# Optimization experiments

Hardware: AMD Instinct MI355X
Metric: run time of the kernel (lower is better)

The kernel has to match this reference:

```python
import jax, jax.numpy as jnp
import numpy as np

N = 50000      # num_nodes
E = 800000     # edges (before self loops)
IN = 64        # in_dim
H = 128        # hidden_node_dim
DH = 256       # decoder_and_message_hidden_dim
L = 3          # propagation_steps


def _lin(key, fan_in, fan_out):
    s = 1.0 / np.sqrt(fan_in)
    return jax.random.uniform(key, (fan_in, fan_out), jnp.float32, -s, s)


def setup_inputs() -> dict:
    key = jax.random.key(0)
    ks = iter(jax.random.split(key, 40))
    x = jax.random.normal(next(ks), (N, IN), jnp.float32)
    edge_index = jax.random.randint(next(ks), (2, E), 0, N, jnp.int64)
    enc_W = _lin(next(ks), IN, H); enc_b = jnp.zeros((H,), jnp.float32)
    # message MLP: Linear(2H->DH) tanh, Linear(DH->DH) tanh, Linear(DH->H)
    msg_W0 = jnp.stack([_lin(next(ks), 2 * H, DH) for _ in range(L)])
    msg_b0 = jnp.zeros((L, DH), jnp.float32)
    msg_W1 = jnp.stack([_lin(next(ks), DH, DH) for _ in range(L)])
    msg_b1 = jnp.zeros((L, DH), jnp.float32)
    msg_W2 = jnp.stack([_lin(next(ks), DH, H) for _ in range(L)])
    msg_b2 = jnp.zeros((L, H), jnp.float32)
    # GRUCell params, torch layout [3H, H] chunks (r, z, n)
    gru_Wih = jnp.stack([_lin(next(ks), H, 3 * H).T for _ in range(L)])
    gru_Whh = jnp.stack([_lin(next(ks), H, 3 * H).T for _ in range(L)])
    gru_bih = jnp.zeros((L, 3 * H), jnp.float32)
    gru_bhh = jnp.zeros((L, 3 * H), jnp.float32)
    # decoder: Linear(H->DH) tanh, Linear(DH->DH) tanh, Linear(DH->1)
    dec_W0 = _lin(next(ks), H, DH); dec_b0 = jnp.zeros((DH,), jnp.float32)
    dec_W1 = _lin(next(ks), DH, DH); dec_b1 = jnp.zeros((DH,), jnp.float32)
    dec_W2 = _lin(next(ks), DH, 1); dec_b2 = jnp.zeros((1,), jnp.float32)
    return dict(x=x, edge_index=edge_index, enc_W=enc_W, enc_b=enc_b,
                msg_W0=msg_W0, msg_b0=msg_b0, msg_W1=msg_W1, msg_b1=msg_b1,
                msg_W2=msg_W2, msg_b2=msg_b2, gru_Wih=gru_Wih, gru_Whh=gru_Whh,
                gru_bih=gru_bih, gru_bhh=gru_bhh, dec_W0=dec_W0, dec_b0=dec_b0,
                dec_W1=dec_W1, dec_b1=dec_b1, dec_W2=dec_W2, dec_b2=dec_b2)


def reference(x, edge_index, enc_W, enc_b, msg_W0, msg_b0, msg_W1, msg_b1,
              msg_W2, msg_b2, gru_Wih, gru_Whh, gru_bih, gru_bhh,
              dec_W0, dec_b0, dec_W1, dec_b1, dec_W2, dec_b2):
    n = x.shape[0]
    # add self loops (PyG add_self_loops appends (v, v))
    loops = jnp.arange(n, dtype=edge_index.dtype)
    src = jnp.concatenate([edge_index[0], loops])  # j (source)
    dst = jnp.concatenate([edge_index[1], loops])  # i (target)
    counts = jax.ops.segment_sum(jnp.ones_like(dst, jnp.float32), dst, num_segments=n)
    h = jnp.tanh(x @ enc_W + enc_b)                # encoder [N, H]
    for l in range(L):
        # message: f([x_i || x_j]) per edge
        m = jnp.concatenate([h[dst], h[src]], axis=-1)            # [E+N, 2H]
        m = jnp.tanh(m @ msg_W0[l] + msg_b0[l])
        m = jnp.tanh(m @ msg_W1[l] + msg_b1[l])
        m = m @ msg_W2[l] + msg_b2[l]                              # [E+N, H]
        aggr = jax.ops.segment_sum(m, dst, num_segments=n) / counts[:, None]
        # GRUCell(input=aggr, hidden=h)
        gi = aggr @ gru_Wih[l].T + gru_bih[l]                      # [N, 3H]
        gh = h @ gru_Whh[l].T + gru_bhh[l]
        i_r, i_z, i_n = jnp.split(gi, 3, axis=-1)
        h_r, h_z, h_n = jnp.split(gh, 3, axis=-1)
        r = jax.nn.sigmoid(i_r + h_r)
        z = jax.nn.sigmoid(i_z + h_z)
        nn_ = jnp.tanh(i_n + r * h_n)
        h = (1.0 - z) * nn_ + z * h
    # decoder
    y = jnp.tanh(h @ dec_W0 + dec_b0)
    y = jnp.tanh(y @ dec_W1 + dec_b1)
    y = y @ dec_W2 + dec_b2                                        # [N, 1]
    return y.reshape(-1, n)[0]                                     # view(-1, N).squeeze(0)
```

## Files before the change

### kernel.cpp

```cpp
#include <hip/hip_runtime.h>

typedef __bf16 bf16x8 __attribute__((ext_vector_type(8)));
typedef float  f32x4  __attribute__((ext_vector_type(4)));

__device__ inline unsigned short f2bf(float f){
  unsigned int u = __float_as_uint(f);
  return (unsigned short)((u + 0x7fffu + ((u >> 16) & 1u)) >> 16);
}
__device__ inline float tanh_fast(float x){
  float e = __builtin_amdgcn_exp2f(x * 2.8853900817779268f);
  return 1.0f - 2.0f * __builtin_amdgcn_rcpf(e + 1.0f);
}
__device__ inline float sigmoid_fast(float x){
  float e = __builtin_amdgcn_exp2f(x * -1.4426950408889634f);
  return __builtin_amdgcn_rcpf(1.0f + e);
}
__device__ inline float bflo(unsigned int u){ return __uint_as_float(u << 16); }
__device__ inline float bfhi(unsigned int u){ return __uint_as_float(u & 0xffff0000u); }

__global__ void k_count(const int* __restrict__ ei, int* __restrict__ cnt, int E){
  int e = blockIdx.x * 256 + threadIdx.x;
  if (e < E) atomicAdd(&cnt[ei[E + e]], 1);
}

__global__ __launch_bounds__(1024) void k_scan(const int* __restrict__ cnt, int* __restrict__ cursor, int N){
  __shared__ int partial[1024];
  int t = threadIdx.x;
  int chunk = (N + 1023) / 1024;
  int lo = t * chunk, hi = min(lo + chunk, N);
  int s = 0;
  for (int v = lo; v < hi; v++) s += cnt[v] + 1;
  partial[t] = s;
  __syncthreads();
  for (int off = 1; off < 1024; off <<= 1){
    int val = (t >= off) ? partial[t - off] : 0;
    __syncthreads();
    partial[t] += val;
    __syncthreads();
  }
  int base = (t == 0) ? 0 : partial[t - 1];
  for (int v = lo; v < hi; v++){ cursor[v] = base; base += cnt[v] + 1; }
}

__global__ void k_scatter(const int* __restrict__ ei, int* __restrict__ cursor,
                          int* __restrict__ srcS, int* __restrict__ dstS, int E, int N){
  int i = blockIdx.x * 256 + threadIdx.x;
  int Et = E + N;
  if (i >= Et) return;
  int s, d;
  if (i < E){ s = ei[i]; d = ei[E + i]; } else { s = d = i - E; }
  int pos = atomicAdd(&cursor[d], 1);
  srcS[pos] = s; dstS[pos] = d;
}

__global__ void k_wprep(const float* __restrict__ msgW1, const float* __restrict__ msgW2,
                        unsigned short* __restrict__ W1T, unsigned short* __restrict__ W2T){
  int idx = blockIdx.x * 256 + threadIdx.x;
  if (idx < 3 * 256 * 256){
    int l = idx >> 16, r = idx & 65535; int n = r >> 8, k = r & 255;
    W1T[idx] = f2bf(msgW1[(size_t)l * 65536 + k * 256 + n]);
  }
  int i2 = idx - 3 * 65536;
  if (i2 >= 0 && i2 < 3 * 128 * 256){
    int l = i2 >> 15, r = i2 & 32767; int hh = r >> 8, k = r & 255;
    W2T[i2] = f2bf(msgW2[(size_t)l * 32768 + k * 128 + hh]);
  }
}

__global__ void k_wprep2(const float* __restrict__ msgW0, unsigned short* __restrict__ W0T){
  int idx = blockIdx.x * 256 + threadIdx.x;
  if (idx >= 3 * 2 * 256 * 128) return;
  int l = idx / 65536, r = idx % 65536;
  int half = r >> 15, r2 = r & 32767, c = r2 >> 7, k = r2 & 127;
  W0T[idx] = f2bf(msgW0[(size_t)l * 65536 + (half * 128 + k) * 256 + c]);
}

__global__ void k_wprep3(const float* __restrict__ gWih, const float* __restrict__ gWhh,
                         unsigned short* __restrict__ Wcat){
  int idx = blockIdx.x * 256 + threadIdx.x;
  if (idx >= 3 * 384 * 256) return;
  int l = idx / 98304, r = idx % 98304, j = r >> 8, k = r & 255;
  float v = (k < 128) ? gWih[((size_t)l * 384 + j) * 128 + k]
                      : gWhh[((size_t)l * 384 + j) * 128 + (k - 128)];
  Wcat[idx] = f2bf(v);
}

__global__ void k_wprep4(const float* __restrict__ encW, const float* __restrict__ dW0,
                         const float* __restrict__ dW1,
                         const float* __restrict__ gbih, const float* __restrict__ gbhh,
                         unsigned short* __restrict__ encWT, unsigned short* __restrict__ dW0T,
                         unsigned short* __restrict__ dW1T,
                         float* __restrict__ brz, float* __restrict__ bin, float* __restrict__ bhn){
  int idx = blockIdx.x * 256 + threadIdx.x;
  if (idx < 8192){ int c = idx >> 6, k = idx & 63; encWT[idx] = f2bf(encW[k * 128 + c]); return; }
  idx -= 8192;
  if (idx < 32768){ int c = idx >> 7, k = idx & 127; dW0T[idx] = f2bf(dW0[k * 256 + c]); return; }
  idx -= 32768;
  if (idx < 65536){ int c = idx >> 8, k = idx & 255; dW1T[idx] = f2bf(dW1[k * 256 + c]); return; }
  idx -= 65536;
  if (idx < 768){ int l = idx >> 8, j = idx & 255; brz[idx] = gbih[l * 384 + j] + gbhh[l * 384 + j]; return; }
  idx -= 768;
  if (idx < 384){ int l = idx >> 7, j = idx & 127; bin[idx] = gbih[l * 384 + 256 + j]; return; }
  idx -= 384;
  if (idx < 384){ int l = idx >> 7, j = idx & 127; bhn[idx] = gbhh[l * 384 + 256 + j]; return; }
}

__global__ __launch_bounds__(256) void k_enc(const float* __restrict__ x,
        const unsigned short* __restrict__ encWT, const float* __restrict__ encb,
        float* __restrict__ h, unsigned short* __restrict__ hb, int N){
  __shared__ __align__(16) unsigned char xb[64 * 128];
  int n0 = blockIdx.x * 64, t = threadIdx.x;
  #pragma unroll
  for (int p = 0; p < 2; p++){
    int i = t + p * 256;
    int row = i >> 3, ch = i & 7;
    int node = n0 + row;
    unsigned int o[4] = {0,0,0,0};
    if (node < N){
      const float* s = x + (size_t)node * 64 + ch * 8;
      float4 a = *(const float4*)s, b = *(const float4*)(s + 4);
      o[0] = (unsigned)f2bf(a.x) | ((unsigned)f2bf(a.y) << 16);
      o[1] = (unsigned)f2bf(a.z) | ((unsigned)f2bf(a.w) << 16);
      o[2] = (unsigned)f2bf(b.x) | ((unsigned)f2bf(b.y) << 16);
      o[3] = (unsigned)f2bf(b.z) | ((unsigned)f2bf(b.w) << 16);
    }
    *(uint4*)(xb + row * 128 + ((ch * 16) ^ ((row & 7) << 4))) = make_uint4(o[0], o[1], o[2], o[3]);
  }
  __syncthreads();
  int wv = t >> 6, lane = t & 63, l15 = lane & 15, kg = lane >> 4;
  f32x4 zero = {0.f, 0.f, 0.f, 0.f};
  f32x4 acc[2][4];
  #pragma unroll
  for (int a_ = 0; a_ < 2; a_++)
    #pragma unroll
    for (int b_ = 0; b_ < 4; b_++) acc[a_][b_] = zero;
  int c32 = wv * 32;
  const unsigned char* wp = (const unsigned char*)encWT;
  #pragma unroll
  for (int ks = 0; ks < 2; ks++){
    int koff = ks * 64 + kg * 16;
    bf16x8 bfr[4], afr[2];
    #pragma unroll
    for (int nt = 0; nt < 4; nt++){
      int row = nt * 16 + l15;
      bfr[nt] = *(const bf16x8*)(xb + row * 128 + (koff ^ ((row & 7) << 4)));
    }
    #pragma unroll
    for (int ct = 0; ct < 2; ct++)
      afr[ct] = *(const bf16x8*)(wp + (size_t)(c32 + ct * 16 + l15) * 128 + koff);
    #pragma unroll
    for (int ct = 0; ct < 2; ct++)
      #pragma unroll
      for (int nt = 0; nt < 4; nt++)
        acc[ct][nt] = __builtin_amdgcn_mfma_f32_16x16x32_bf16(afr[ct], bfr[nt], acc[ct][nt], 0, 0, 0);
  }
  #pragma unroll
  for (int ct = 0; ct < 2; ct++){
    int c = c32 + ct * 16 + kg * 4;
    float4 be = *(const float4*)(encb + c);
    #pragma unroll
    for (int nt = 0; nt < 4; nt++){
      int node = n0 + nt * 16 + l15;
      if (node >= N) continue;
      f32x4 v = acc[ct][nt];
      float o0 = tanh_fast(v[0] + be.x), o1 = tanh_fast(v[1] + be.y);
      float o2 = tanh_fast(v[2] + be.z), o3 = tanh_fast(v[3] + be.w);
      float4 fo; fo.x = o0; fo.y = o1; fo.z = o2; fo.w = o3;
      *(float4*)(h + (size_t)node * 128 + c) = fo;
      uint2 bo;
      bo.x = (unsigned)f2bf(o0) | ((unsigned)f2bf(o1) << 16);
      bo.y = (unsigned)f2bf(o2) | ((unsigned)f2bf(o3) << 16);
      *(uint2*)(hb + (size_t)node * 128 + c) = bo;
    }
  }
}

__global__ __launch_bounds__(256) void k_ab(const unsigned short* __restrict__ hb,
        const unsigned short* __restrict__ W0T,
        unsigned short* __restrict__ A, unsigned short* __restrict__ B, int N){
  __shared__ __align__(16) unsigned char ub[64 * 256];
  int n0 = blockIdx.x * 64, t = threadIdx.x;
  #pragma unroll
  for (int p = 0; p < 4; p++){
    int i = t + p * 256;
    int row = i >> 4, ch = i & 15;
    int node = n0 + row;
    uint4 v = (node < N) ? *(const uint4*)(hb + (size_t)node * 128 + ch * 8) : make_uint4(0,0,0,0);
    *(uint4*)(ub + row * 256 + ((ch * 16) ^ ((row & 7) << 4))) = v;
  }
  __syncthreads();
  int wv = t >> 6, lane = t & 63, l15 = lane & 15, kg = lane >> 4;
  f32x4 zero = {0.f, 0.f, 0.f, 0.f};
  f32x4 accA[4][4], accB[4][4];
  #pragma unroll
  for (int a_ = 0; a_ < 4; a_++)
    #pragma unroll
    for (int b_ = 0; b_ < 4; b_++){ accA[a_][b_] = zero; accB[a_][b_] = zero; }
  int c64 = wv * 64;
  const unsigned char* wa = (const unsigned char*)W0T;
  const unsigned char* wb = wa + 65536;
  #pragma unroll
  for (int ks = 0; ks < 4; ks++){
    int koff = ks * 64 + kg * 16;
    bf16x8 bfr[4];
    #pragma unroll
    for (int nt = 0; nt < 4; nt++){
      int row = nt * 16 + l15;
      bfr[nt] = *(const bf16x8*)(ub + row * 256 + (koff ^ ((row & 7) << 4)));
    }
    bf16x8 afA[4], afB[4];
    #pragma unroll
    for (int ct = 0; ct < 4; ct++){
      int r = c64 + ct * 16 + l15;
      afA[ct] = *(const bf16x8*)(wa + (size_t)r * 256 + koff);
      afB[ct] = *(const bf16x8*)(wb + (size_t)r * 256 + koff);
    }
    #pragma unroll
    for (int ct = 0; ct < 4; ct++)
      #pragma unroll
      for (int nt = 0; nt < 4; nt++){
        accA[ct][nt] = __builtin_amdgcn_mfma_f32_16x16x32_bf16(afA[ct], bfr[nt], accA[ct][nt], 0, 0, 0);
        accB[ct][nt] = __builtin_amdgcn_mfma_f32_16x16x32_bf16(afB[ct], bfr[nt], accB[ct][nt], 0, 0, 0);
      }
  }
  #pragma unroll
  for (int ct = 0; ct < 4; ct++){
    int c = c64 + ct * 16 + kg * 4;
    #pragma unroll
    for (int nt = 0; nt < 4; nt++){
      int node = n0 + nt * 16 + l15;
      if (node >= N) continue;
      f32x4 va = accA[ct][nt], vb = accB[ct][nt];
      uint2 oa, ob;
      oa.x = (unsigned)f2bf(va[0]) | ((unsigned)f2bf(va[1]) << 16);
      oa.y = (unsigned)f2bf(va[2]) | ((unsigned)f2bf(va[3]) << 16);
      ob.x = (unsigned)f2bf(vb[0]) | ((unsigned)f2bf(vb[1]) << 16);
      ob.y = (unsigned)f2bf(vb[2]) | ((unsigned)f2bf(vb[3]) << 16);
      *(uint2*)(A + (size_t)node * 256 + c) = oa;
      *(uint2*)(B + (size_t)node * 256 + c) = ob;
    }
  }
}

__global__ __launch_bounds__(256) void k_edge(
        const int* __restrict__ srcS, const int* __restrict__ dstS,
        const unsigned short* __restrict__ Abuf, const unsigned short* __restrict__ Bbuf,
        const unsigned short* __restrict__ W1T, const unsigned short* __restrict__ W2T,
        const float* __restrict__ b0, const float* __restrict__ b1, const float* __restrict__ b2,
        float* __restrict__ aggr){
  __shared__ __align__(16) unsigned char smem[64 * 512];
  __shared__ __align__(16) unsigned char t1[64 * 512];
  __shared__ int dIdx[64], sIdx[64];
  __shared__ int segStart[64];
  __shared__ int nsegS, endAllS;
  unsigned char* t0 = smem;
  int t  = threadIdx.x;
  int e0 = blockIdx.x * 64;
  if (t < 64){
    int e = e0 + t;
    sIdx[t] = srcS[e]; dIdx[t] = dstS[e];
  }
  __syncthreads();
  if (t < 64){
    int d = dIdx[t];
    bool valid = (d >= 0);
    bool flag  = valid && (t == 0 || dIdx[t] != dIdx[t-1]);
    unsigned long long startMask = __ballot(flag);
    unsigned long long invMask   = __ballot(!valid);
    if (flag){
      int s = __popcll(startMask & ((1ull << t) - 1ull));
      segStart[s] = t;
    }
    if (t == 0){
      nsegS   = (int)__popcll(startMask);
      endAllS = 64 - (int)__popcll(invMask);
    }
  }
  {
    int chunk = t & 31;
    int rbase = t >> 5;
    uint4 av[8], bv[8];
    #pragma unroll
    for (int p = 0; p < 8; p++){
      int row = p*8 + rbase;
      int d = dIdx[row], s = sIdx[row];
      if (d >= 0){
        av[p] = *(const uint4*)(Abuf + (size_t)d*256 + chunk*8);
        bv[p] = *(const uint4*)(Bbuf + (size_t)s*256 + chunk*8);
      } else {
        av[p] = make_uint4(0,0,0,0); bv[p] = make_uint4(0,0,0,0);
      }
    }
    float bb[8];
    #pragma unroll
    for (int q = 0; q < 8; q++) bb[q] = b0[chunk*8 + q];
    #pragma unroll
    for (int p = 0; p < 8; p++){
      int row = p*8 + rbase;
      bool valid = (dIdx[row] >= 0);
      unsigned int o[4]; unsigned int ua, ub;
      ua = av[p].x; ub = bv[p].x;
      o[0] = (unsigned int)f2bf(tanh_fast(bflo(ua)+bflo(ub)+bb[0])) |
             ((unsigned int)f2bf(tanh_fast(bfhi(ua)+bfhi(ub)+bb[1])) << 16);
      ua = av[p].y; ub = bv[p].y;
      o[1] = (unsigned int)f2bf(tanh_fast(bflo(ua)+bflo(ub)+bb[2])) |
             ((unsigned int)f2bf(tanh_fast(bfhi(ua)+bfhi(ub)+bb[3])) << 16);
      ua = av[p].z; ub = bv[p].z;
      o[2] = (unsigned int)f2bf(tanh_fast(bflo(ua)+bflo(ub)+bb[4])) |
             ((unsigned int)f2bf(tanh_fast(bfhi(ua)+bfhi(ub)+bb[5])) << 16);
      ua = av[p].w; ub = bv[p].w;
      o[3] = (unsigned int)f2bf(tanh_fast(bflo(ua)+bflo(ub)+bb[6])) |
             ((unsigned int)f2bf(tanh_fast(bfhi(ua)+bfhi(ub)+bb[7])) << 16);
      if (!valid){ o[0]=o[1]=o[2]=o[3]=0u; }
      *(uint4*)(t0 + row*512 + ((chunk*16) ^ ((row&7)<<4))) = make_uint4(o[0],o[1],o[2],o[3]);
    }
  }
  __syncthreads();
  int wv = t >> 6, lane = t & 63;
  int l15 = lane & 15, kg = lane >> 4;
  {
    f32x4 zero = {0.f, 0.f, 0.f, 0.f};
    f32x4 acc[4][4];
    #pragma unroll
    for (int a_ = 0; a_ < 4; a_++)
      #pragma unroll
      for (int b_ = 0; b_ < 4; b_++) acc[a_][b_] = zero;
    int nbase = wv * 64;
    const unsigned char* w1b = (const unsigned char*)W1T;
    #pragma unroll
    for (int ks = 0; ks < 8; ks++){
      int koff = ks*64 + kg*16;
      bf16x8 afr[4], bfr[4];
      #pragma unroll
      for (int nt = 0; nt < 4; nt++)
        afr[nt] = *(const bf16x8*)(w1b + (size_t)(nbase + nt*16 + l15)*512 + koff);
      #pragma unroll
      for (int et = 0; et < 4; et++){
        int row = et*16 + l15;
        bfr[et] = *(const bf16x8*)(t0 + row*512 + (koff ^ ((row&7)<<4)));
      }
      #pragma unroll
      for (int nt = 0; nt < 4; nt++)
        #pragma unroll
        for (int et = 0; et < 4; et++)
          acc[nt][et] = __builtin_amdgcn_mfma_f32_16x16x32_bf16(afr[nt], bfr[et], acc[nt][et], 0, 0, 0);
    }
    #pragma unroll
    for (int nt = 0; nt < 4; nt++){
      int nb2 = nbase + nt*16 + kg*4;
      float c0 = b1[nb2], c1 = b1[nb2+1], c2 = b1[nb2+2], c3 = b1[nb2+3];
      #pragma unroll
      for (int et = 0; et < 4; et++){
        int edge = et*16 + l15;
        f32x4 v = acc[nt][et];
        unsigned int p0 = (unsigned int)f2bf(tanh_fast(v[0]+c0)) |
                          ((unsigned int)f2bf(tanh_fast(v[1]+c1)) << 16);
        unsigned int p1 = (unsigned int)f2bf(tanh_fast(v[2]+c2)) |
                          ((unsigned int)f2bf(tanh_fast(v[3]+c3)) << 16);
        *(uint2*)(t1 + edge*512 + ((nb2*2) ^ ((edge&7)<<4))) = make_uint2(p0, p1);
      }
    }
  }
  __syncthreads();
  {
    f32x4 zero = {0.f, 0.f, 0.f, 0.f};
    f32x4 acc2[2][4];
    #pragma unroll
    for (int a_ = 0; a_ < 2; a_++)
      #pragma unroll
      for (int b_ = 0; b_ < 4; b_++) acc2[a_][b_] = zero;
    int hbase = wv * 32;
    const unsigned char* w2b = (const unsigned char*)W2T;
    #pragma unroll
    for (int ks = 0; ks < 8; ks++){
      int koff = ks*64 + kg*16;
      bf16x8 afr[2], bfr[4];
      #pragma unroll
      for (int ht = 0; ht < 2; ht++)
        afr[ht] = *(const bf16x8*)(w2b + (size_t)(hbase + ht*16 + l15)*512 + koff);
      #pragma unroll
      for (int et = 0; et < 4; et++){
        int row = et*16 + l15;
        bfr[et] = *(const bf16x8*)(t1 + row*512 + (koff ^ ((row&7)<<4)));
      }
      #pragma unroll
      for (int ht = 0; ht < 2; ht++)
        #pragma unroll
        for (int et = 0; et < 4; et++)
          acc2[ht][et] = __builtin_amdgcn_mfma_f32_16x16x32_bf16(afr[ht], bfr[et], acc2[ht][et], 0, 0, 0);
    }
    #pragma unroll
    for (int ht = 0; ht < 2; ht++){
      int hb_ = hbase + ht*16 + kg*4;
      float c0 = b2[hb_], c1 = b2[hb_+1], c2 = b2[hb_+2], c3 = b2[hb_+3];
      int cch = hb_ >> 2;
      #pragma unroll
      for (int et = 0; et < 4; et++){
        int edge = et*16 + l15;
        f32x4 v = acc2[ht][et];
        float4 o; o.x = v[0]+c0; o.y = v[1]+c1; o.z = v[2]+c2; o.w = v[3]+c3;
        *(float4*)(smem + edge*512 + ((cch ^ (edge&7)) << 4)) = o;
      }
    }
  }
  __syncthreads();
  {
    int c    = t & 31;
    int sstr = t >> 5;
    int nseg = nsegS, endAll = endAllS;
    for (int s = sstr; s < nseg; s += 8){
      int st = segStart[s];
      int en = (s + 1 < nseg) ? segStart[s + 1] : endAll;
      int d  = dIdx[st];
      float4 sum; sum.x = sum.y = sum.z = sum.w = 0.f;
      for (int e = st; e < en; e++){
        float4 v = *(const float4*)(smem + e*512 + ((c ^ (e&7)) << 4));
        sum.x += v.x; sum.y += v.y; sum.z += v.z; sum.w += v.w;
      }
      float* base = aggr + (size_t)d*128 + c*4;
      atomicAdd(base+0, sum.x);
      atomicAdd(base+1, sum.y);
      atomicAdd(base+2, sum.z);
      atomicAdd(base+3, sum.w);
    }
  }
}

__global__ __launch_bounds__(256) void k_gru(const float* __restrict__ aggr, const int* __restrict__ cnt,
    float* __restrict__ h, unsigned short* __restrict__ hb,
    const unsigned short* __restrict__ Wcat, const float* __restrict__ brz,
    const float* __restrict__ bin, const float* __restrict__ bhn, int N){
  __shared__ __align__(16) unsigned char u[64 * 512];
  __shared__ __align__(16) unsigned char hf[64 * 512];
  int n0 = blockIdx.x * 64, t = threadIdx.x;
  {
    int row = t >> 2, node = n0 + row;
    int q4 = t & 3;
    bool isA = q4 < 2;
    float inv = 0.f;
    if (isA && node < N) inv = __builtin_amdgcn_rcpf((float)(cnt[node] + 1));
    #pragma unroll
    for (int p = 0; p < 8; p++){
      int ch = q4 * 8 + p;
      unsigned int o[4] = {0,0,0,0};
      if (node < N){
        if (isA){
          const float* s = aggr + (size_t)node * 128 + ch * 8;
          float4 a = *(const float4*)s, b = *(const float4*)(s + 4);
          a.x *= inv; a.y *= inv; a.z *= inv; a.w *= inv;
          b.x *= inv; b.y *= inv; b.z *= inv; b.w *= inv;
          o[0] = (unsigned)f2bf(a.x) | ((unsigned)f2bf(a.y) << 16);
          o[1] = (unsigned)f2bf(a.z) | ((unsigned)f2bf(a.w) << 16);
          o[2] = (unsigned)f2bf(b.x) | ((unsigned)f2bf(b.y) << 16);
          o[3] = (unsigned)f2bf(b.z) | ((unsigned)f2bf(b.w) << 16);
        } else {
          const float* s = h + (size_t)node * 128 + (ch - 16) * 8;
          float4 a = *(const float4*)s, b = *(const float4*)(s + 4);
          o[0] = (unsigned)f2bf(a.x) | ((unsigned)f2bf(a.y) << 16);
          o[1] = (unsigned)f2bf(a.z) | ((unsigned)f2bf(a.w) << 16);
          o[2] = (unsigned)f2bf(b.x) | ((unsigned)f2bf(b.y) << 16);
          o[3] = (unsigned)f2bf(b.z) | ((unsigned)f2bf(b.w) << 16);
          int c2 = (ch - 16) * 2;
          *(float4*)(hf + row * 512 + ((c2 * 16) ^ ((row & 7) << 4))) = a;
          *(float4*)(hf + row * 512 + (((c2 + 1) * 16) ^ ((row & 7) << 4))) = b;
        }
      }
      *(uint4*)(u + row * 512 + ((ch * 16) ^ ((row & 7) << 4))) = make_uint4(o[0], o[1], o[2], o[3]);
    }
  }
  __syncthreads();
  int wv = t >> 6, lane = t & 63, l15 = lane & 15, kg = lane >> 4;
  int j32 = wv * 32;
  f32x4 zero = {0.f, 0.f, 0.f, 0.f};
  f32x4 accR[2][4], accZ[2][4], accI[2][4], accH[2][4];
  #pragma unroll
  for (int a_ = 0; a_ < 2; a_++)
    #pragma unroll
    for (int b_ = 0; b_ < 4; b_++){ accR[a_][b_] = zero; accZ[a_][b_] = zero; accI[a_][b_] = zero; accH[a_][b_] = zero; }
  const unsigned char* wc = (const unsigned char*)Wcat;
  #pragma unroll
  for (int ks = 0; ks < 8; ks++){
    int koff = ks * 64 + kg * 16;
    bf16x8 bfr[4];
    #pragma unroll
    for (int nt = 0; nt < 4; nt++){
      int row = nt * 16 + l15;
      bfr[nt] = *(const bf16x8*)(u + row * 512 + (koff ^ ((row & 7) << 4)));
    }
    bf16x8 aR[2], aZ[2], aN[2];
    #pragma unroll
    for (int jt = 0; jt < 2; jt++){
      int jr = j32 + jt * 16 + l15;
      aR[jt] = *(const bf16x8*)(wc + (size_t)jr * 512 + koff);
      aZ[jt] = *(const bf16x8*)(wc + (size_t)(128 + jr) * 512 + koff);
      aN[jt] = *(const bf16x8*)(wc + (size_t)(256 + jr) * 512 + koff);
    }
    #pragma unroll
    for (int jt = 0; jt < 2; jt++)
      #pragma unroll
      for (int nt = 0; nt < 4; nt++){
        accR[jt][nt] = __builtin_amdgcn_mfma_f32_16x16x32_bf16(aR[jt], bfr[nt], accR[jt][nt], 0, 0, 0);
        accZ[jt][nt] = __builtin_amdgcn_mfma_f32_16x16x32_bf16(aZ[jt], bfr[nt], accZ[jt][nt], 0, 0, 0);
      }
    if (ks < 4){
      #pragma unroll
      for (int jt = 0; jt < 2; jt++)
        #pragma unroll
        for (int nt = 0; nt < 4; nt++)
          accI[jt][nt] = __builtin_amdgcn_mfma_f32_16x16x32_bf16(aN[jt], bfr[nt], accI[jt][nt], 0, 0, 0);
    } else {
      #pragma unroll
      for (int jt = 0; jt < 2; jt++)
        #pragma unroll
        for (int nt = 0; nt < 4; nt++)
          accH[jt][nt] = __builtin_amdgcn_mfma_f32_16x16x32_bf16(aN[jt], bfr[nt], accH[jt][nt], 0, 0, 0);
    }
  }
  #pragma unroll
  for (int jt = 0; jt < 2; jt++){
    int j = j32 + jt * 16 + kg * 4;
    float4 br = *(const float4*)(brz + j);
    float4 bz = *(const float4*)(brz + 128 + j);
    float4 bi = *(const float4*)(bin + j);
    float4 bh = *(const float4*)(bhn + j);
    #pragma unroll
    for (int nt = 0; nt < 4; nt++){
      int rloc = nt * 16 + l15;
      int node = n0 + rloc;
      if (node >= N) continue;
      float4 hold = *(const float4*)(hf + rloc * 512 + ((j * 4) ^ ((rloc & 7) << 4)));
      f32x4 vr = accR[jt][nt], vz = accZ[jt][nt], vi = accI[jt][nt], vh = accH[jt][nt];
      float o[4];
      {
        float r0 = sigmoid_fast(vr[0] + br.x), z0 = sigmoid_fast(vz[0] + bz.x);
        o[0] = (1.f - z0) * tanh_fast(vi[0] + bi.x + r0 * (vh[0] + bh.x)) + z0 * hold.x;
        float r1 = sigmoid_fast(vr[1] + br.y), z1 = sigmoid_fast(vz[1] + bz.y);
        o[1] = (1.f - z1) * tanh_fast(vi[1] + bi.y + r1 * (vh[1] + bh.y)) + z1 * hold.y;
        float r2 = sigmoid_fast(vr[2] + br.z), z2 = sigmoid_fast(vz[2] + bz.z);
        o[2] = (1.f - z2) * tanh_fast(vi[2] + bi.z + r2 * (vh[2] + bh.z)) + z2 * hold.z;
        float r3 = sigmoid_fast(vr[3] + br.w), z3 = sigmoid_fast(vz[3] + bz.w);
        o[3] = (1.f - z3) * tanh_fast(vi[3] + bi.w + r3 * (vh[3] + bh.w)) + z3 * hold.w;
      }
      float4 fo; fo.x = o[0]; fo.y = o[1]; fo.z = o[2]; fo.w = o[3];
      *(float4*)(h + (size_t)node * 128 + j) = fo;
      uint2 bo;
      bo.x = (unsigned)f2bf(o[0]) | ((unsigned)f2bf(o[1]) << 16);
      bo.y = (unsigned)f2bf(o[2]) | ((unsigned)f2bf(o[3]) << 16);
      *(uint2*)(hb + (size_t)node * 128 + j) = bo;
    }
  }
}

__global__ __launch_bounds__(256) void k_dec(const unsigned short* __restrict__ hb,
    const unsigned short* __restrict__ dW0T, const float* __restrict__ db0,
    const unsigned short* __restrict__ dW1T, const float* __restrict__ db1,
    const float* __restrict__ dW2, const float* __restrict__ db2,
    float* __restrict__ out, int N){
  __shared__ __align__(16) unsigned char ub[64 * 256];
  __shared__ __align__(16) unsigned char y1[64 * 512];
  __shared__ __align__(16) unsigned char y2[64 * 1024];
  int n0 = blockIdx.x * 64, t = threadIdx.x;
  #pragma unroll
  for (int p = 0; p < 4; p++){
    int i = t + p * 256;
    int row = i >> 4, ch = i & 15;
    int node = n0 + row;
    uint4 v = (node < N) ? *(const uint4*)(hb + (size_t)node * 128 + ch * 8) : make_uint4(0,0,0,0);
    *(uint4*)(ub + row * 256 + ((ch * 16) ^ ((row & 7) << 4))) = v;
  }
  __syncthreads();
  int wv = t >> 6, lane = t & 63, l15 = lane & 15, kg = lane >> 4;
  f32x4 zero = {0.f, 0.f, 0.f, 0.f};
  int c64 = wv * 64;
  {
    f32x4 acc[4][4];
    #pragma unroll
    for (int a_ = 0; a_ < 4; a_++)
      #pragma unroll
      for (int b_ = 0; b_ < 4; b_++) acc[a_][b_] = zero;
    const unsigned char* wp = (const unsigned char*)dW0T;
    #pragma unroll
    for (int ks = 0; ks < 4; ks++){
      int koff = ks * 64 + kg * 16;
      bf16x8 bfr[4], afr[4];
      #pragma unroll
      for (int nt = 0; nt < 4; nt++){
        int row = nt * 16 + l15;
        bfr[nt] = *(const bf16x8*)(ub + row * 256 + (koff ^ ((row & 7) << 4)));
      }
      #pragma unroll
      for (int ct = 0; ct < 4; ct++)
        afr[ct] = *(const bf16x8*)(wp + (size_t)(c64 + ct * 16 + l15) * 256 + koff);
      #pragma unroll
      for (int ct = 0; ct < 4; ct++)
        #pragma unroll
        for (int nt = 0; nt < 4; nt++)
          acc[ct][nt] = __builtin_amdgcn_mfma_f32_16x16x32_bf16(afr[ct], bfr[nt], acc[ct][nt], 0, 0, 0);
    }
    #pragma unroll
    for (int ct = 0; ct < 4; ct++){
      int c = c64 + ct * 16 + kg * 4;
      float4 b4 = *(const float4*)(db0 + c);
      #pragma unroll
      for (int nt = 0; nt < 4; nt++){
        int row = nt * 16 + l15;
        f32x4 v = acc[ct][nt];
        unsigned int p0 = (unsigned)f2bf(tanh_fast(v[0] + b4.x)) | ((unsigned)f2bf(tanh_fast(v[1] + b4.y)) << 16);
        unsigned int p1 = (unsigned)f2bf(tanh_fast(v[2] + b4.z)) | ((unsigned)f2bf(tanh_fast(v[3] + b4.w)) << 16);
        *(uint2*)(y1 + row * 512 + ((c * 2) ^ ((row & 7) << 4))) = make_uint2(p0, p1);
      }
    }
  }
  __syncthreads();
  {
    f32x4 acc[4][4];
    #pragma unroll
    for (int a_ = 0; a_ < 4; a_++)
      #pragma unroll
      for (int b_ = 0; b_ < 4; b_++) acc[a_][b_] = zero;
    const unsigned char* wp = (const unsigned char*)dW1T;
    #pragma unroll
    for (int ks = 0; ks < 8; ks++){
      int koff = ks * 64 + kg * 16;
      bf16x8 bfr[4], afr[4];
      #pragma unroll
      for (int nt = 0; nt < 4; nt++){
        int row = nt * 16 + l15;
        bfr[nt] = *(const bf16x8*)(y1 + row * 512 + (koff ^ ((row & 7) << 4)));
      }
      #pragma unroll
      for (int ct = 0; ct < 4; ct++)
        afr[ct] = *(const bf16x8*)(wp + (size_t)(c64 + ct * 16 + l15) * 512 + koff);
      #pragma unroll
      for (int ct = 0; ct < 4; ct++)
        #pragma unroll
        for (int nt = 0; nt < 4; nt++)
          acc[ct][nt] = __builtin_amdgcn_mfma_f32_16x16x32_bf16(afr[ct], bfr[nt], acc[ct][nt], 0, 0, 0);
    }
    #pragma unroll
    for (int ct = 0; ct < 4; ct++){
      int c = c64 + ct * 16 + kg * 4;
      float4 b4 = *(const float4*)(db1 + c);
      #pragma unroll
      for (int nt = 0; nt < 4; nt++){
        int row = nt * 16 + l15;
        f32x4 v = acc[ct][nt];
        float4 o;
        o.x = tanh_fast(v[0] + b4.x); o.y = tanh_fast(v[1] + b4.y);
        o.z = tanh_fast(v[2] + b4.z); o.w = tanh_fast(v[3] + b4.w);
        *(float4*)(y2 + row * 1024 + ((c * 4) ^ ((row & 7) << 4))) = o;
      }
    }
  }
  __syncthreads();
  {
    int node = t >> 2, part = t & 3;
    float p = 0.f;
    #pragma unroll
    for (int q = 0; q < 16; q++){
      int c = part * 64 + q * 4;
      float4 v = *(const float4*)(y2 + node * 1024 + ((c * 4) ^ ((node & 7) << 4)));
      float4 w = *(const float4*)(dW2 + c);
      p += v.x * w.x + v.y * w.y + v.z * w.z + v.w * w.w;
    }
    p += __shfl_down(p, 2, 4);
    p += __shfl_down(p, 1, 4);
    if (part == 0 && (n0 + node) < N) out[n0 + node] = p + db2[0];
  }
}

extern "C" void kernel_launch(void* const* d_in, const int* in_sizes, int n_in,
                              void* d_out, int out_size, void* d_ws, size_t ws_size,
                              hipStream_t stream){
  const float* x     = (const float*)d_in[0];
  const int*   ei    = (const int*)  d_in[1];
  const float* encW  = (const float*)d_in[2];
  const float* encb  = (const float*)d_in[3];
  const float* msgW0 = (const float*)d_in[4];
  const float* msgb0 = (const float*)d_in[5];
  const float* msgW1 = (const float*)d_in[6];
  const float* msgb1 = (const float*)d_in[7];
  const float* msgW2 = (const float*)d_in[8];
  const float* msgb2 = (const float*)d_in[9];
  const float* gWih  = (const float*)d_in[10];
  const float* gWhh  = (const float*)d_in[11];
  const float* gbih  = (const float*)d_in[12];
  const float* gbhh  = (const float*)d_in[13];
  const float* dW0   = (const float*)d_in[14];
  const float* db0   = (const float*)d_in[15];
  const float* dW1   = (const float*)d_in[16];
  const float* db1   = (const float*)d_in[17];
  const float* dW2   = (const float*)d_in[18];
  const float* db2   = (const float*)d_in[19];
  int N = in_sizes[0] / 64;
  int E = in_sizes[1] / 2;
  float* out = (float*)d_out;

  int Et = E + N;
  int EtPad = (Et + 63) & ~63;

  char* ws = (char*)d_ws;
  size_t off = 0;
  auto alloc = [&](size_t bytes)->void*{
    void* p = ws + off; off += (bytes + 255) & ~(size_t)255; return p;
  };
  float*          h      = (float*)         alloc((size_t)N * 128 * 4);
  unsigned short* hbuf   = (unsigned short*)alloc((size_t)N * 128 * 2);
  unsigned short* Abuf   = (unsigned short*)alloc((size_t)N * 256 * 2);
  unsigned short* Bbuf   = (unsigned short*)alloc((size_t)N * 256 * 2);
  float*          aggr   = (float*)         alloc((size_t)N * 128 * 4);
  int*            cnt    = (int*)           alloc((size_t)N * 4);
  int*            cursor = (int*)           alloc((size_t)N * 4);
  int*            srcS   = (int*)           alloc((size_t)EtPad * 4);
  int*            dstS   = (int*)           alloc((size_t)EtPad * 4);
  unsigned short* W1T    = (unsigned short*)alloc((size_t)3 * 65536 * 2);
  unsigned short* W2T    = (unsigned short*)alloc((size_t)3 * 32768 * 2);
  unsigned short* W0T    = (unsigned short*)alloc((size_t)3 * 65536 * 2);
  unsigned short* Wcat   = (unsigned short*)alloc((size_t)3 * 98304 * 2);
  unsigned short* encWT  = (unsigned short*)alloc((size_t)8192 * 2);
  unsigned short* dW0T   = (unsigned short*)alloc((size_t)32768 * 2);
  unsigned short* dW1T   = (unsigned short*)alloc((size_t)65536 * 2);
  float*          brz    = (float*)         alloc((size_t)768 * 4);
  float*          binb   = (float*)         alloc((size_t)384 * 4);
  float*          bhnb   = (float*)         alloc((size_t)384 * 4);
  (void)ws_size; (void)n_in; (void)out_size;

  hipMemsetAsync(cnt, 0, (size_t)N * 4, stream);
  hipMemsetAsync(dstS, 0xFF, (size_t)EtPad * 4, stream);
  k_count<<<(E + 255) / 256, 256, 0, stream>>>(ei, cnt, E);
  k_scan<<<1, 1024, 0, stream>>>(cnt, cursor, N);
  k_scatter<<<(Et + 255) / 256, 256, 0, stream>>>(ei, cursor, srcS, dstS, E, N);
  k_wprep<<<(3 * 65536 + 3 * 32768 + 255) / 256, 256, 0, stream>>>(msgW1, msgW2, W1T, W2T);
  k_wprep2<<<(3 * 65536 + 255) / 256, 256, 0, stream>>>(msgW0, W0T);
  k_wprep3<<<(3 * 98304 + 255) / 256, 256, 0, stream>>>(gWih, gWhh, Wcat);
  k_wprep4<<<(108032 + 255) / 256, 256, 0, stream>>>(encW, dW0, dW1, gbih, gbhh,
                                                     encWT, dW0T, dW1T, brz, binb, bhnb);

  int nb64 = (N + 63) / 64;
  k_enc<<<nb64, 256, 0, stream>>>(x, encWT, encb, h, hbuf, N);

  int eb = EtPad / 64;
  for (int l = 0; l < 3; l++){
    k_ab<<<nb64, 256, 0, stream>>>(hbuf, W0T + (size_t)l * 65536, Abuf, Bbuf, N);
    hipMemsetAsync(aggr, 0, (size_t)N * 128 * 4, stream);
    k_edge<<<eb, 256, 0, stream>>>(srcS, dstS, Abuf, Bbuf,
        W1T + (size_t)l * 65536, W2T + (size_t)l * 32768,
        msgb0 + (size_t)l * 256, msgb1 + (size_t)l * 256, msgb2 + (size_t)l * 128,
        aggr);
    k_gru<<<nb64, 256, 0, stream>>>(aggr, cnt, h, hbuf,
        Wcat + (size_t)l * 98304, brz + (size_t)l * 256,
        binb + (size_t)l * 128, bhnb + (size_t)l * 128, N);
  }
  k_dec<<<nb64, 256, 0, stream>>>(hbuf, dW0T, db0, dW1T, db1, dW2, db2, out, N);
}
```

Measured before the change: 1.796 ms.

## Make edge kernel persistent over four tiles with prefetched gathers

The edge-message kernel now runs 512 threads per block and processes four 64-edge tiles in sequence. Each tile's A/B row gathers are issued before the current tile is computed, so global gather latency overlaps with the MFMA and tanh work. Full __syncthreads are replaced by an LDS-only wait plus s_barrier. Work per wave is halved, so register pressure drops and more waves fit per CU. In exchange there are four barriers per tile, and weights are reloaded from global memory or cache for every tile.

```diff
diff --git a/kernel.cpp b/kernel.cpp
--- a/kernel.cpp
+++ b/kernel.cpp
@@ -17,6 +17,11 @@
 }
 __device__ inline float bflo(unsigned int u){ return __uint_as_float(u << 16); }
 __device__ inline float bfhi(unsigned int u){ return __uint_as_float(u & 0xffff0000u); }
+
+__device__ __forceinline__ void bar_nodrain(){
+  asm volatile("s_waitcnt lgkmcnt(0)" ::: "memory");
+  __builtin_amdgcn_s_barrier();
+}
 
 __global__ void k_count(const int* __restrict__ ei, int* __restrict__ cnt, int E){
   int e = blockIdx.x * 256 + threadIdx.x;
@@ -242,7 +247,7 @@
   }
 }
 
-__global__ __launch_bounds__(256) void k_edge(
+__global__ __launch_bounds__(512, 4) void k_edge(
         const int* __restrict__ srcS, const int* __restrict__ dstS,
         const unsigned short* __restrict__ Abuf, const unsigned short* __restrict__ Bbuf,
         const unsigned short* __restrict__ W1T, const unsigned short* __restrict__ W2T,
@@ -250,179 +255,184 @@
         float* __restrict__ aggr){
   __shared__ __align__(16) unsigned char smem[64 * 512];
   __shared__ __align__(16) unsigned char t1[64 * 512];
-  __shared__ int dIdx[64], sIdx[64];
-  __shared__ int segStart[64];
-  __shared__ int nsegS, endAllS;
+  __shared__ int sIdx[256], dIdx[256];
+  __shared__ int segStart[4][64];
+  __shared__ int nsegS[4], endAllS[4];
   unsigned char* t0 = smem;
-  int t  = threadIdx.x;
-  int e0 = blockIdx.x * 64;
-  if (t < 64){
-    int e = e0 + t;
-    sIdx[t] = srcS[e]; dIdx[t] = dstS[e];
-  }
+  int t = threadIdx.x;
+  int e0 = blockIdx.x * 256;
+  if (t < 256){ sIdx[t] = srcS[e0 + t]; dIdx[t] = dstS[e0 + t]; }
   __syncthreads();
-  if (t < 64){
-    int d = dIdx[t];
+  int wv = t >> 6, lane = t & 63, l15 = lane & 15, kg = lane >> 4;
+  if (wv < 4){
+    int d = dIdx[wv * 64 + lane];
     bool valid = (d >= 0);
-    bool flag  = valid && (t == 0 || dIdx[t] != dIdx[t-1]);
+    bool flag  = valid && (lane == 0 || dIdx[wv * 64 + lane - 1] != d);
     unsigned long long startMask = __ballot(flag);
     unsigned long long invMask   = __ballot(!valid);
     if (flag){
-      int s = __popcll(startMask & ((1ull << t) - 1ull));
-      segStart[s] = t;
-    }
-    if (t == 0){
-      nsegS   = (int)__popcll(startMask);
-      endAllS = 64 - (int)__popcll(invMask);
-    }
-  }
-  {
-    int chunk = t & 31;
-    int rbase = t >> 5;
-    uint4 av[8], bv[8];
-    #pragma unroll
-    for (int p = 0; p < 8; p++){
-      int row = p*8 + rbase;
-      int d = dIdx[row], s = sIdx[row];
+      int s = __popcll(startMask & ((1ull << lane) - 1ull));
+      segStart[wv][s] = lane;
+    }
+    if (lane == 0){
+      nsegS[wv]   = (int)__popcll(startMask);
+      endAllS[wv] = 64 - (int)__popcll(invMask);
+    }
+  }
+  int chunk = t & 31, rgrp = t >> 5;
+  float bb[8];
+  #pragma unroll
+  for (int q = 0; q < 8; q++) bb[q] = b0[chunk * 8 + q];
+
+  int nbase = wv * 32;
+  float c1r[2][4];
+  #pragma unroll
+  for (int nt = 0; nt < 2; nt++){
+    int nb2 = nbase + nt * 16 + kg * 4;
+    c1r[nt][0] = b1[nb2]; c1r[nt][1] = b1[nb2+1]; c1r[nt][2] = b1[nb2+2]; c1r[nt][3] = b1[nb2+3];
+  }
+  int hbase = wv * 16;
+  int hb_ = hbase + kg * 4;
+  float c20 = b2[hb_], c21 = b2[hb_+1], c22 = b2[hb_+2], c23 = b2[hb_+3];
+
+  uint4 av0[4], bv0[4], av1[4], bv1[4];
+  auto issue = [&](int T, uint4* av, uint4* bv){
+    #pragma unroll
+    for (int p = 0; p < 4; p++){
+      int r = p * 16 + rgrp;
+      int d = dIdx[T * 64 + r], s = sIdx[T * 64 + r];
       if (d >= 0){
-        av[p] = *(const uint4*)(Abuf + (size_t)d*256 + chunk*8);
-        bv[p] = *(const uint4*)(Bbuf + (size_t)s*256 + chunk*8);
-      } else {
-        av[p] = make_uint4(0,0,0,0); bv[p] = make_uint4(0,0,0,0);
-      }
-    }
-    float bb[8];
-    #pragma unroll
-    for (int q = 0; q < 8; q++) bb[q] = b0[chunk*8 + q];
-    #pragma unroll
-    for (int p = 0; p < 8; p++){
-      int row = p*8 + rbase;
-      bool valid = (dIdx[row] >= 0);
+        av[p] = *(const uint4*)(Abuf + (size_t)d * 256 + chunk * 8);
+        bv[p] = *(const uint4*)(Bbuf + (size_t)s * 256 + chunk * 8);
+      } else { av[p] = make_uint4(0,0,0,0); bv[p] = make_uint4(0,0,0,0); }
+    }
+  };
+  issue(0, av0, bv0);
+
+  const unsigned char* w1b = (const unsigned char*)W1T;
+  const unsigned char* w2b = (const unsigned char*)W2T;
+  f32x4 zero = {0.f, 0.f, 0.f, 0.f};
+
+  #pragma unroll
+  for (int T = 0; T < 4; T++){
+    uint4* avc = (T & 1) ? av1 : av0;
+    uint4* bvc = (T & 1) ? bv1 : bv0;
+    uint4* avn = (T & 1) ? av0 : av1;
+    uint4* bvn = (T & 1) ? bv0 : bv1;
+    if (T < 3) issue(T + 1, avn, bvn);
+
+    #pragma unroll
+    for (int p = 0; p < 4; p++){
+      int r = p * 16 + rgrp;
+      bool valid = (dIdx[T * 64 + r] >= 0);
       unsigned int o[4]; unsigned int ua, ub;
-      ua = av[p].x; ub = bv[p].x;
-      o[0] = (unsigned int)f2bf(tanh_fast(bflo(ua)+bflo(ub)+bb[0])) |
-             ((unsigned int)f2bf(tanh_fast(bfhi(ua)+bfhi(ub)+bb[1])) << 16);
-      ua = av[p].y; ub = bv[p].y;
-      o[1] = (unsigned int)f2bf(tanh_fast(bflo(ua)+bflo(ub)+bb[2])) |
-             ((unsigned int)f2bf(tanh_fast(bfhi(ua)+bfhi(ub)+bb[3])) << 16);
-      ua = av[p].z; ub = bv[p].z;
-      o[2] = (unsigned int)f2bf(tanh_fast(bflo(ua)+bflo(ub)+bb[4])) |
-             ((unsigned int)f2bf(tanh_fast(bfhi(ua)+bfhi(ub)+bb[5])) << 16);
-      ua = av[p].w; ub = bv[p].w;
-      o[3] = (unsigned int)f2bf(tanh_fast(bflo(ua)+bflo(ub)+bb[6])) |
-             ((unsigned int)f2bf(tanh_fast(bfhi(ua)+bfhi(ub)+bb[7])) << 16);
+      ua = avc[p].x; ub = bvc[p].x;
+      o[0] = (unsigned)f2bf(tanh_fast(bflo(ua)+bflo(ub)+bb[0])) |
+             ((unsigned)f2bf(tanh_fast(bfhi(ua)+bfhi(ub)+bb[1])) << 16);
+      ua = avc[p].y; ub = bvc[p].y;
+      o[1] = (unsigned)f2bf(tanh_fast(bflo(ua)+bflo(ub)+bb[2])) |
+             ((unsigned)f2bf(tanh_fast(bfhi(ua)+bfhi(ub)+bb[3])) << 16);
+      ua = avc[p].z; ub = bvc[p].z;
+      o[2] = (unsigned)f2bf(tanh_fast(bflo(ua)+bflo(ub)+bb[4])) |
+             ((unsigned)f2bf(tanh_fast(bfhi(ua)+bfhi(ub)+bb[5])) << 16);
+      ua = avc[p].w; ub = bvc[p].w;
+      o[3] = (unsigned)f2bf(tanh_fast(bflo(ua)+bflo(ub)+bb[6])) |
+             ((unsigned)f2bf(tanh_fast(bfhi(ua)+bfhi(ub)+bb[7])) << 16);
       if (!valid){ o[0]=o[1]=o[2]=o[3]=0u; }
-      *(uint4*)(t0 + row*512 + ((chunk*16) ^ ((row&7)<<4))) = make_uint4(o[0],o[1],o[2],o[3]);
-    }
-  }
-  __syncthreads();
-  int wv = t >> 6, lane = t & 63;
-  int l15 = lane & 15, kg = lane >> 4;
-  {
-    f32x4 zero = {0.f, 0.f, 0.f, 0.f};
-    f32x4 acc[4][4];
-    #pragma unroll
-    for (int a_ = 0; a_ < 4; a_++)
-      #pragma unroll
-      for (int b_ = 0; b_ < 4; b_++) acc[a_][b_] = zero;
-    int nbase = wv * 64;
-    const unsigned char* w1b = (const unsigned char*)W1T;
-    #pragma unroll
-    for (int ks = 0; ks < 8; ks++){
-      int koff = ks*64 + kg*16;
-      bf16x8 afr[4], bfr[4];
-      #pragma unroll
-      for (int nt = 0; nt < 4; nt++)
-        afr[nt] = *(const bf16x8*)(w1b + (size_t)(nbase + nt*16 + l15)*512 + koff);
+      *(uint4*)(t0 + r * 512 + ((chunk * 16) ^ ((r & 7) << 4))) = make_uint4(o[0],o[1],o[2],o[3]);
+    }
+    bar_nodrain();
+
+    {
+      f32x4 acc[2][4];
+      #pragma unroll
+      for (int a_ = 0; a_ < 2; a_++)
+        #pragma unroll
+        for (int b_ = 0; b_ < 4; b_++) acc[a_][b_] = zero;
+      #pragma unroll
+      for (int ks = 0; ks < 8; ks++){
+        int koff = ks * 64 + kg * 16;
+        bf16x8 afr[2], bfr[4];
+        #pragma unroll
+        for (int nt = 0; nt < 2; nt++)
+          afr[nt] = *(const bf16x8*)(w1b + (size_t)(nbase + nt * 16 + l15) * 512 + koff);
+        #pragma unroll
+        for (int et = 0; et < 4; et++){
+          int row = et * 16 + l15;
+          bfr[et] = *(const bf16x8*)(t0 + row * 512 + (koff ^ ((row & 7) << 4)));
+        }
+        #pragma unroll
+        for (int nt = 0; nt < 2; nt++)
+          #pragma unroll
+          for (int et = 0; et < 4; et++)
+            acc[nt][et] = __builtin_amdgcn_mfma_f32_16x16x32_bf16(afr[nt], bfr[et], acc[nt][et], 0, 0, 0);
+      }
+      #pragma unroll
+      for (int nt = 0; nt < 2; nt++){
+        int nb2 = nbase + nt * 16 + kg * 4;
+        #pragma unroll
+        for (int et = 0; et < 4; et++){
+          int edge = et * 16 + l15;
+          f32x4 v = acc[nt][et];
+          unsigned int p0 = (unsigned)f2bf(tanh_fast(v[0] + c1r[nt][0])) |
+                            ((unsigned)f2bf(tanh_fast(v[1] + c1r[nt][1])) << 16);
+          unsigned int p1 = (unsigned)f2bf(tanh_fast(v[2] + c1r[nt][2])) |
+                            ((unsigned)f2bf(tanh_fast(v[3] + c1r[nt][3])) << 16);
+          *(uint2*)(t1 + edge * 512 + ((nb2 * 2) ^ ((edge & 7) << 4))) = make_uint2(p0, p1);
+        }
+      }
+    }
+    bar_nodrain();
+
+    {
+      f32x4 acc2[4];
+      #pragma unroll
+      for (int b_ = 0; b_ < 4; b_++) acc2[b_] = zero;
+      #pragma unroll
+      for (int ks = 0; ks < 8; ks++){
+        int koff = ks * 64 + kg * 16;
+        bf16x8 afr = *(const bf16x8*)(w2b + (size_t)(hbase + l15) * 512 + koff);
+        bf16x8 bfr[4];
+        #pragma unroll
+        for (int et = 0; et < 4; et++){
+          int row = et * 16 + l15;
+          bfr[et] = *(const bf16x8*)(t1 + row * 512 + (koff ^ ((row & 7) << 4)));
+        }
+        #pragma unroll
+        for (int et = 0; et < 4; et++)
+          acc2[et] = __builtin_amdgcn_mfma_f32_16x16x32_bf16(afr, bfr[et], acc2[et], 0, 0, 0);
+      }
+      int cch = hb_ >> 2;
       #pragma unroll
       for (int et = 0; et < 4; et++){
-        int row = et*16 + l15;
-        bfr[et] = *(const bf16x8*)(t0 + row*512 + (koff ^ ((row&7)<<4)));
-      }
-      #pragma unroll
-      for (int nt = 0; nt < 4; nt++)
-        #pragma unroll
-        for (int et = 0; et < 4; et++)
-          acc[nt][et] = __builtin_amdgcn_mfma_f32_16x16x32_bf16(afr[nt], bfr[et], acc[nt][et], 0, 0, 0);
-    }
-    #pragma unroll
-    for (int nt = 0; nt < 4; nt++){
-      int nb2 = nbase + nt*16 + kg*4;
-      float c0 = b1[nb2], c1 = b1[nb2+1], c2 = b1[nb2+2], c3 = b1[nb2+3];
-      #pragma unroll
-      for (int et = 0; et < 4; et++){
-        int edge = et*16 + l15;
-        f32x4 v = acc[nt][et];
-        unsigned int p0 = (unsigned int)f2bf(tanh_fast(v[0]+c0)) |
-                          ((unsigned int)f2bf(tanh_fast(v[1]+c1)) << 16);
-        unsigned int p1 = (unsigned int)f2bf(tanh_fast(v[2]+c2)) |
-                          ((unsigned int)f2bf(tanh_fast(v[3]+c3)) << 16);
-        *(uint2*)(t1 + edge*512 + ((nb2*2) ^ ((edge&7)<<4))) = make_uint2(p0, p1);
-      }
-    }
-  }
-  __syncthreads();
-  {
-    f32x4 zero = {0.f, 0.f, 0.f, 0.f};
-    f32x4 acc2[2][4];
-    #pragma unroll
-    for (int a_ = 0; a_ < 2; a_++)
-      #pragma unroll
-      for (int b_ = 0; b_ < 4; b_++) acc2[a_][b_] = zero;
-    int hbase = wv * 32;
-    const unsigned char* w2b = (const unsigned char*)W2T;
-    #pragma unroll
-    for (int ks = 0; ks < 8; ks++){
-      int koff = ks*64 + kg*16;
-      bf16x8 afr[2], bfr[4];
-      #pragma unroll
-      for (int ht = 0; ht < 2; ht++)
-        afr[ht] = *(const bf16x8*)(w2b + (size_t)(hbase + ht*16 + l15)*512 + koff);
-      #pragma unroll
-      for (int et = 0; et < 4; et++){
-        int row = et*16 + l15;
-        bfr[et] = *(const bf16x8*)(t1 + row*512 + (koff ^ ((row&7)<<4)));
-      }
-      #pragma unroll
-      for (int ht = 0; ht < 2; ht++)
-        #pragma unroll
-        for (int et = 0; et < 4; et++)
-          acc2[ht][et] = __builtin_amdgcn_mfma_f32_16x16x32_bf16(afr[ht], bfr[et], acc2[ht][et], 0, 0, 0);
-    }
-    #pragma unroll
-    for (int ht = 0; ht < 2; ht++){
-      int hb_ = hbase + ht*16 + kg*4;
-      float c0 = b2[hb_], c1 = b2[hb_+1], c2 = b2[hb_+2], c3 = b2[hb_+3];
-      int cch = hb_ >> 2;
-      #pragma unroll
-      for (int et = 0; et < 4; et++){
-        int edge = et*16 + l15;
-        f32x4 v = acc2[ht][et];
-        float4 o; o.x = v[0]+c0; o.y = v[1]+c1; o.z = v[2]+c2; o.w = v[3]+c3;
-        *(float4*)(smem + edge*512 + ((cch ^ (edge&7)) << 4)) = o;
-      }
-    }
-  }
-  __syncthreads();
-  {
-    int c    = t & 31;
-    int sstr = t >> 5;
-    int nseg = nsegS, endAll = endAllS;
-    for (int s = sstr; s < nseg; s += 8){
-      int st = segStart[s];
-      int en = (s + 1 < nseg) ? segStart[s + 1] : endAll;
-      int d  = dIdx[st];
-      float4 sum; sum.x = sum.y = sum.z = sum.w = 0.f;
-      for (int e = st; e < en; e++){
-        float4 v = *(const float4*)(smem + e*512 + ((c ^ (e&7)) << 4));
-        sum.x += v.x; sum.y += v.y; sum.z += v.z; sum.w += v.w;
-      }
-      float* base = aggr + (size_t)d*128 + c*4;
-      atomicAdd(base+0, sum.x);
-      atomicAdd(base+1, sum.y);
-      atomicAdd(base+2, sum.z);
-      atomicAdd(base+3, sum.w);
-    }
+        int edge = et * 16 + l15;
+        f32x4 v = acc2[et];
+        float4 o; o.x = v[0]+c20; o.y = v[1]+c21; o.z = v[2]+c22; o.w = v[3]+c23;
+        *(float4*)(smem + edge * 512 + ((cch ^ (edge & 7)) << 4)) = o;
+      }
+    }
+    bar_nodrain();
+
+    {
+      int c = t & 31, sstr = t >> 5;
+      int nseg = nsegS[T], endAll = endAllS[T];
+      for (int s = sstr; s < nseg; s += 16){
+        int st = segStart[T][s];
+        int en = (s + 1 < nseg) ? segStart[T][s + 1] : endAll;
+        int d  = dIdx[T * 64 + st];
+        float4 sum; sum.x = sum.y = sum.z = sum.w = 0.f;
+        for (int e = st; e < en; e++){
+          float4 v = *(const float4*)(smem + e * 512 + ((c ^ (e & 7)) << 4));
+          sum.x += v.x; sum.y += v.y; sum.z += v.z; sum.w += v.w;
+        }
+        float* base = aggr + (size_t)d * 128 + c * 4;
+        atomicAdd(base + 0, sum.x);
+        atomicAdd(base + 1, sum.y);
+        atomicAdd(base + 2, sum.z);
+        atomicAdd(base + 3, sum.w);
+      }
+    }
+    bar_nodrain();
   }
 }
 
@@ -697,7 +707,7 @@
   float* out = (float*)d_out;
 
   int Et = E + N;
-  int EtPad = (Et + 63) & ~63;
+  int EtPad = (Et + 255) & ~255;
 
   char* ws = (char*)d_ws;
   size_t off = 0;
@@ -739,11 +749,11 @@
   int nb64 = (N + 63) / 64;
   k_enc<<<nb64, 256, 0, stream>>>(x, encWT, encb, h, hbuf, N);
 
-  int eb = EtPad / 64;
+  int eb = EtPad / 256;
   for (int l = 0; l < 3; l++){
     k_ab<<<nb64, 256, 0, stream>>>(hbuf, W0T + (size_t)l * 65536, Abuf, Bbuf, N);
     hipMemsetAsync(aggr, 0, (size_t)N * 128 * 4, stream);
-    k_edge<<<eb, 256, 0, stream>>>(srcS, dstS, Abuf, Bbuf,
+    k_edge<<<eb, 512, 0, stream>>>(srcS, dstS, Abuf, Bbuf,
         W1T + (size_t)l * 65536, W2T + (size_t)l * 32768,
         msgb0 + (size_t)l * 256, msgb1 + (size_t)l * 256, msgb2 + (size_t)l * 128,
         aggr);
```

Result: slower. 2.120 ms (+18.0%).
